# Optimization experiments

Measured on AMD Instinct MI355X. Metric: run time of the kernel, lower is better.

The kernel has to match this reference:

```python
import jax, jax.numpy as jnp
import numpy as np

B, S, E, H = 4, 2048, 1024, 16
DH = E // H  # head_dim = 64


def setup_inputs() -> dict:
    key = jax.random.key(0)
    k1, k2, k3 = jax.random.split(key, 3)
    x = jax.random.normal(k1, (B, S, E), dtype=jnp.float32)
    # xavier-uniform-like scale for dense kernels
    Wqkv = jax.random.normal(k2, (E, 3 * E), dtype=jnp.float32) * (1.0 / np.sqrt(E))
    Wout = jax.random.normal(k3, (E, E), dtype=jnp.float32) * (1.0 / np.sqrt(E))
    return {"x": x, "Wqkv": Wqkv, "Wout": Wout}


def reference(x, Wqkv, Wout):
    b, s, e = x.shape
    qkv = jnp.einsum("bse,ef->bsf", x, Wqkv)            # [B,S,3E]
    qkv = qkv.reshape(b, s, H, 3 * DH).transpose(0, 2, 1, 3)  # [B,H,S,3*DH]
    q, k, v = jnp.split(qkv, 3, axis=-1)                # each [B,H,S,DH]
    scale = 1.0 / jnp.sqrt(jnp.asarray(DH, dtype=x.dtype))
    scores = jnp.einsum("bhqd,bhkd->bhqk", q, k) * scale  # [B,H,S,S] materialized
    attn = jax.nn.softmax(scores, axis=-1)
    values = jnp.einsum("bhqk,bhkd->bhqd", attn, v)     # [B,H,S,DH]
    values = values.transpose(0, 2, 1, 3).reshape(b, s, e)
    out = jnp.einsum("bse,ef->bsf", values, Wout)       # [B,S,E]
    return out
```

## Files before the change

### kernel.cpp

```cpp
#include <hip/hip_runtime.h>

typedef __attribute__((ext_vector_type(8))) __bf16 bf16x8;
typedef __attribute__((ext_vector_type(4))) float f32x4;

#define LOG2E 1.4426950408889634f
#define QSCALE (0.125f * LOG2E)

static __device__ __forceinline__ void gl_lds16(const void* g, void* l) {
  __builtin_amdgcn_global_load_lds(
      (__attribute__((address_space(1))) void*)(g),
      (__attribute__((address_space(3))) void*)(l), 16, 0, 0);
}

__global__ __launch_bounds__(256) void convert_f32_bf16(const float* __restrict__ in,
                                                        __bf16* __restrict__ out,
                                                        int n8) {
  const int i = blockIdx.x * 256 + threadIdx.x;
  if (i >= n8) return;
  const f32x4 a = *(const f32x4*)(in + (size_t)i * 8);
  const f32x4 b = *(const f32x4*)(in + (size_t)i * 8 + 4);
  bf16x8 o;
#pragma unroll
  for (int j = 0; j < 4; ++j) o[j] = (__bf16)a[j];
#pragma unroll
  for (int j = 0; j < 4; ++j) o[4 + j] = (__bf16)b[j];
  *(bf16x8*)(out + (size_t)i * 8) = o;
}

__global__ __launch_bounds__(256) void transpose_f32_bf16(
    const float* __restrict__ in, __bf16* __restrict__ out, int R, int C) {
  __shared__ __bf16 tile[64][72];
  const int t = threadIdx.x;
  const int c0 = blockIdx.x * 64;
  const int r0 = blockIdx.y * 64;
  const int lr = t >> 2;
  const int lc = (t & 3) * 16;
  const float* src = in + (size_t)(r0 + lr) * C + c0 + lc;
  bf16x8 w0, w1;
#pragma unroll
  for (int j = 0; j < 2; ++j) {
    const f32x4 a = *(const f32x4*)(src + j * 8);
    const f32x4 b = *(const f32x4*)(src + j * 8 + 4);
    bf16x8 o;
#pragma unroll
    for (int k = 0; k < 4; ++k) o[k] = (__bf16)a[k];
#pragma unroll
    for (int k = 0; k < 4; ++k) o[4 + k] = (__bf16)b[k];
    *(bf16x8*)&tile[lr][lc + j * 8] = o;
  }
  __syncthreads();
#pragma unroll
  for (int j = 0; j < 8; ++j) {
    w0[j] = tile[lc + j][lr];
    w1[j] = tile[lc + 8 + j][lr];
  }
  __bf16* dst = out + (size_t)(c0 + lr) * R + r0 + lc;
  *(bf16x8*)dst = w0;
  *(bf16x8*)(dst + 8) = w1;
}


#define STAGE_A(TT, KH)                                                  \
  do {                                                                   \
    const int kg_ = (TT) * 64 + (KH) * 32;                               \
    char* d_ = lds + ((TT) & 1) * 32768 + (KH) * 16384 + t * 16;         \
    gl_lds16(Ab + g0 + kg_, d_);                                         \
    gl_lds16(Ab + g1 + kg_, d_ + 8192);                                  \
  } while (0)

#define STAGE_B(TT, KH)                                                  \
  do {                                                                   \
    const int kg_ = (TT) * 64 + (KH) * 32;                               \
    char* d_ = lds + 65536 + ((TT) & 1) * 16384 + (KH) * 8192 + t * 16;  \
    gl_lds16(Bb + g0 + kg_, d_);                                         \
  } while (0)

#define READ_AB(KK)                                                              \
  do {                                                                           \
    const char* pa_ = lds + buf * 32768 + (KK) * 16384 + wm * 8192 + lfo;        \
    a0 = *(const bf16x8*)pa_;                                                    \
    a1 = *(const bf16x8*)(pa_ + 1024);                                           \
    a2 = *(const bf16x8*)(pa_ + 2048);                                           \
    a3 = *(const bf16x8*)(pa_ + 3072);                                           \
    a4 = *(const bf16x8*)(pa_ + 4096);                                           \
    a5 = *(const bf16x8*)(pa_ + 5120);                                           \
    a6 = *(const bf16x8*)(pa_ + 6144);                                           \
    a7 = *(const bf16x8*)(pa_ + 7168);                                           \
    const char* pb_ = lds + 65536 + buf * 16384 + (KK) * 8192 + wn * 2048 + lfo; \
    b0 = *(const bf16x8*)pb_;                                                    \
    b1 = *(const bf16x8*)(pb_ + 1024);                                           \
  } while (0)

#define MROW(MI, AV)                                                             \
  acc[MI][0] = __builtin_amdgcn_mfma_f32_16x16x32_bf16(AV, b0, acc[MI][0], 0, 0, 0); \
  acc[MI][1] = __builtin_amdgcn_mfma_f32_16x16x32_bf16(AV, b1, acc[MI][1], 0, 0, 0);

#define MFMA16()                       \
  do {                                 \
    __builtin_amdgcn_s_setprio(1);     \
    MROW(0, a0)                        \
    MROW(1, a1)                        \
    MROW(2, a2)                        \
    MROW(3, a3)                        \
    MROW(4, a4)                        \
    MROW(5, a5)                        \
    MROW(6, a6)                        \
    MROW(7, a7)                        \
    __builtin_amdgcn_s_setprio(0);     \
  } while (0)

template <int EPI>
__global__ __launch_bounds__(512, 2) void gemm256(
    const __bf16* __restrict__ A, const __bf16* __restrict__ Bt,
    float* __restrict__ Cf, __bf16* __restrict__ q_ws, __bf16* __restrict__ k_ws,
    __bf16* __restrict__ vT_ws, int M, int N, int K) {
  (void)M;
  extern __shared__ char lds[];
  const int t = threadIdx.x;
  const int lane = t & 63;
  const int quad = lane >> 4, l15 = lane & 15;
  const int w = t >> 6;
  const int wm = w >> 2, wn = w & 3;

  const int olid = blockIdx.y * gridDim.x + blockIdx.x;
  const int xcd = olid & 7, loc = olid >> 3;
  const int m0 = (xcd * 4 + (loc & 3)) * 256;
  const int n0 = (loc >> 2) * 128;

  int rowS[2], kcS[2];
#pragma unroll
  for (int l = 0; l < 2; ++l) {
    const int LB = l * 8192 + t * 16;
    const int r_in = (LB >> 6) & 15;
    const int ch = ((LB >> 5) & 1) ^ ((r_in >> 3) & 1);
    rowS[l] = (LB >> 10) * 16 + r_in;
    kcS[l] = ch * 16 + ((LB >> 4) & 1) * 8;
  }
  const __bf16* Ab = A + (size_t)m0 * K;
  const __bf16* Bb = Bt + (size_t)n0 * K;
  const size_t g0 = (size_t)rowS[0] * K + kcS[0];
  const size_t g1 = (size_t)rowS[1] * K + kcS[1];

  const int lfo = l15 * 64 + ((((quad >> 1) ^ (l15 >> 3)) & 1) << 5) + ((quad & 1) << 4);

  const f32x4 fzero = {0.f, 0.f, 0.f, 0.f};
  f32x4 acc[8][2];
#pragma unroll
  for (int i = 0; i < 8; ++i) {
    acc[i][0] = fzero;
    acc[i][1] = fzero;
  }

  const int nt = K >> 6;
  bf16x8 a0, a1, a2, a3, a4, a5, a6, a7, b0, b1;

  STAGE_A(0, 0);
  STAGE_B(0, 0);
  STAGE_A(0, 1);
  STAGE_B(0, 1);
  if (nt > 1) {
    STAGE_A(1, 0);
    STAGE_B(1, 0);
    asm volatile("s_waitcnt vmcnt(3)");
  } else {
    asm volatile("s_waitcnt vmcnt(0)");
  }
  __builtin_amdgcn_s_barrier();

  for (int tt = 0; tt < nt; ++tt) {
    const int buf = tt & 1;
    READ_AB(0);
    if (tt + 1 < nt) {
      STAGE_A(tt + 1, 1);
      STAGE_B(tt + 1, 1);
    }
    __builtin_amdgcn_s_barrier();
    asm volatile("s_waitcnt lgkmcnt(0)");
    MFMA16();
    if (tt + 1 < nt)
      asm volatile("s_waitcnt vmcnt(6)");
    else
      asm volatile("s_waitcnt vmcnt(0)");
    __builtin_amdgcn_s_barrier();
    READ_AB(1);
    if (tt + 2 < nt) {
      STAGE_A(tt + 2, 0);
      STAGE_B(tt + 2, 0);
    }
    __builtin_amdgcn_s_barrier();
    asm volatile("s_waitcnt lgkmcnt(0)");
    MFMA16();
    if (tt + 2 < nt)
      asm volatile("s_waitcnt vmcnt(6)");
    else if (tt + 1 < nt)
      asm volatile("s_waitcnt vmcnt(3)");
    else
      asm volatile("s_waitcnt vmcnt(0)");
    __builtin_amdgcn_s_barrier();
  }

#pragma unroll
  for (int mi = 0; mi < 8; ++mi) {
#pragma unroll
    for (int r = 0; r < 4; ++r) {
      const int row = m0 + wm * 128 + mi * 16 + quad * 4 + r;
#pragma unroll
      for (int ni = 0; ni < 2; ++ni) {
        const int col = n0 + wn * 32 + ni * 16 + l15;
        const float v = acc[mi][ni][r];
        if (EPI == 0) {
          const int b = row >> 11, s = row & 2047;
          const int h = col / 192;
          const int rr = col - h * 192;
          const int ty = rr >> 6, d = rr & 63;
          const int bh = b * 16 + h;
          if (ty == 0)
            q_ws[((size_t)bh * 2048 + s) * 64 + d] = (__bf16)(v * QSCALE);
          else if (ty == 1)
            k_ws[((size_t)bh * 2048 + s) * 64 + d] = (__bf16)v;
          else
            vT_ws[((size_t)bh * 64 + d) * 2048 + s] = (__bf16)v;
        } else {
          Cf[(size_t)row * N + col] = v;
        }
      }
    }
  }
}

__global__ __launch_bounds__(256) void flash_attn(
    const __bf16* __restrict__ q_ws, const __bf16* __restrict__ k_ws,
    const __bf16* __restrict__ vT_ws, __bf16* __restrict__ values, int bh0) {
  __shared__ __bf16 sK[64][72];
  __shared__ __bf16 sVt[64][72];
  __shared__ __bf16 sP[4][32][72];
  const int t = threadIdx.x;
  const int lane = t & 63, w = t >> 6, quad = lane >> 4, l15 = lane & 15;
  const int qt = blockIdx.x;
  const int bh = blockIdx.y + bh0;
  const __bf16* Qb = q_ws + (size_t)bh * 2048 * 64;
  const __bf16* Kb = k_ws + (size_t)bh * 2048 * 64;
  const __bf16* Vtb = vT_ws + (size_t)bh * 64 * 2048;
  const int qrow0 = qt * 128 + w * 32;

  bf16x8 qf[2][2];
#pragma unroll
  for (int mi = 0; mi < 2; ++mi)
#pragma unroll
    for (int ks = 0; ks < 2; ++ks)
      qf[mi][ks] = *(const bf16x8*)(Qb + (size_t)(qrow0 + mi * 16 + l15) * 64 +
                                    ks * 32 + quad * 8);

  bf16x8 ones;
#pragma unroll
  for (int j = 0; j < 8; ++j) ones[j] = (__bf16)1.0f;

  const f32x4 fzero = {0.f, 0.f, 0.f, 0.f};
  f32x4 accO[2][4];
  f32x4 accL[2];
#pragma unroll
  for (int mi = 0; mi < 2; ++mi) {
    accL[mi] = fzero;
#pragma unroll
    for (int ni = 0; ni < 4; ++ni) accO[mi][ni] = fzero;
  }

  const int srow = t >> 2;
  const int scol = (t & 3) * 16;

  bf16x8 ka, kb2, va, vb;
  {
    const __bf16* ks0 = Kb + (size_t)srow * 64 + scol;
    ka = *(const bf16x8*)ks0;
    kb2 = *(const bf16x8*)(ks0 + 8);
    const __bf16* vs0 = Vtb + (size_t)srow * 2048 + scol;
    va = *(const bf16x8*)vs0;
    vb = *(const bf16x8*)(vs0 + 8);
  }

  for (int kt = 0; kt < 32; ++kt) {
    *(bf16x8*)&sK[srow][scol] = ka;
    *(bf16x8*)&sK[srow][scol + 8] = kb2;
    *(bf16x8*)&sVt[srow][scol] = va;
    *(bf16x8*)&sVt[srow][scol + 8] = vb;
    __syncthreads();

    if (kt < 31) {
      const __bf16* ksn = Kb + (size_t)((kt + 1) * 64 + srow) * 64 + scol;
      ka = *(const bf16x8*)ksn;
      kb2 = *(const bf16x8*)(ksn + 8);
      const __bf16* vsn = Vtb + (size_t)srow * 2048 + (kt + 1) * 64 + scol;
      va = *(const bf16x8*)vsn;
      vb = *(const bf16x8*)(vsn + 8);
    }

    f32x4 accS[2][4];
#pragma unroll
    for (int mi = 0; mi < 2; ++mi)
#pragma unroll
      for (int ni = 0; ni < 4; ++ni) accS[mi][ni] = fzero;
#pragma unroll
    for (int ks = 0; ks < 2; ++ks) {
      bf16x8 kf[4];
#pragma unroll
      for (int ni = 0; ni < 4; ++ni)
        kf[ni] = *(const bf16x8*)&sK[ni * 16 + l15][ks * 32 + quad * 8];
#pragma unroll
      for (int mi = 0; mi < 2; ++mi)
#pragma unroll
        for (int ni = 0; ni < 4; ++ni)
          accS[mi][ni] = __builtin_amdgcn_mfma_f32_16x16x32_bf16(
              qf[mi][ks], kf[ni], accS[mi][ni], 0, 0, 0);
    }

#pragma unroll
    for (int mi = 0; mi < 2; ++mi) {
#pragma unroll
      for (int r = 0; r < 4; ++r) {
        const int prow = mi * 16 + quad * 4 + r;
#pragma unroll
        for (int ni = 0; ni < 4; ++ni) {
          const float p = __builtin_amdgcn_exp2f(accS[mi][ni][r]);
          sP[w][prow][ni * 16 + l15] = (__bf16)p;
        }
      }
    }
    __threadfence_block();

#pragma unroll
    for (int ks = 0; ks < 2; ++ks) {
      bf16x8 vf[4], pf[2];
#pragma unroll
      for (int ni = 0; ni < 4; ++ni)
        vf[ni] = *(const bf16x8*)&sVt[ni * 16 + l15][ks * 32 + quad * 8];
#pragma unroll
      for (int mi = 0; mi < 2; ++mi)
        pf[mi] = *(const bf16x8*)&sP[w][mi * 16 + l15][ks * 32 + quad * 8];
#pragma unroll
      for (int mi = 0; mi < 2; ++mi) {
#pragma unroll
        for (int ni = 0; ni < 4; ++ni)
          accO[mi][ni] = __builtin_amdgcn_mfma_f32_16x16x32_bf16(
              pf[mi], vf[ni], accO[mi][ni], 0, 0, 0);
        accL[mi] = __builtin_amdgcn_mfma_f32_16x16x32_bf16(pf[mi], ones, accL[mi],
                                                           0, 0, 0);
      }
    }
    __syncthreads();
  }

  const int b = bh >> 4, h = bh & 15;
#pragma unroll
  for (int mi = 0; mi < 2; ++mi) {
#pragma unroll
    for (int r = 0; r < 4; ++r) {
      const float inv = 1.0f / accL[mi][r];
      const int s = qrow0 + mi * 16 + quad * 4 + r;
#pragma unroll
      for (int ni = 0; ni < 4; ++ni)
        values[((size_t)(b * 2048 + s)) * 1024 + h * 64 + ni * 16 + l15] =
            (__bf16)(accO[mi][ni][r] * inv);
    }
  }
}

extern "C" void kernel_launch(void* const* d_in, const int* in_sizes, int n_in,
                              void* d_out, int out_size, void* d_ws, size_t ws_size,
                              hipStream_t stream) {
  (void)out_size; (void)ws_size;
  float* out = (float*)d_out;
  char* wsb = (char*)d_ws;
  __bf16* xb = (__bf16*)(wsb + 256);
  __bf16* WqkvT = xb + 8388608;
  __bf16* WoutT = WqkvT + 3145728;
  __bf16* q_ws = WoutT + 1048576;
  __bf16* k_ws = q_ws + 8388608;
  __bf16* vT_ws = k_ws + 8388608;
  __bf16* values = xb;

  const float *px = (const float*)d_in[0], *pw = (const float*)d_in[1],
              *po = (const float*)d_in[2];
  for (int i = 0; i < n_in; ++i) {
    if (in_sizes[i] == 8388608) px = (const float*)d_in[i];
    else if (in_sizes[i] == 3145728) pw = (const float*)d_in[i];
    else if (in_sizes[i] == 1048576) po = (const float*)d_in[i];
  }

  hipFuncSetAttribute(reinterpret_cast<const void*>(&gemm256<0>),
                      hipFuncAttributeMaxDynamicSharedMemorySize, 98304);
  hipFuncSetAttribute(reinterpret_cast<const void*>(&gemm256<1>),
                      hipFuncAttributeMaxDynamicSharedMemorySize, 98304);

  convert_f32_bf16<<<4096, 256, 0, stream>>>(px, xb, 1048576);
  transpose_f32_bf16<<<dim3(48, 16), 256, 0, stream>>>(pw, WqkvT, 1024, 3072);
  transpose_f32_bf16<<<dim3(16, 16), 256, 0, stream>>>(po, WoutT, 1024, 1024);
  gemm256<0><<<dim3(32, 24), 512, 98304, stream>>>(xb, WqkvT, nullptr, q_ws, k_ws,
                                                   vT_ws, 8192, 3072, 1024);
  flash_attn<<<dim3(16, 64), 256, 0, stream>>>(q_ws, k_ws, vT_ws, values, 0);
  gemm256<1><<<dim3(32, 8), 512, 98304, stream>>>(values, WoutT, out, nullptr,
                                                  nullptr, nullptr, 8192, 1024, 1024);
}
```

Measured before the change: 310.0 us.

## Shrink GEMM tile to 128x128, split attention launch, change sP padding

The GEMM kernel's M tile drops from 256 to 128 rows. Each warp now holds four MFMA rows instead of eight, LDS use falls to 64KB, and the launch bounds ask for 4 blocks per CU, so twice as many blocks run with higher occupancy. The cost is less data reuse per block. Separately, the flash attention launch is split into two launches of 32 heads each. The sP row padding changes from 72 to 68, which alters the LDS bank mapping and could add conflicts or affect alignment.

```diff
diff --git a/kernel.cpp b/kernel.cpp
--- a/kernel.cpp
+++ b/kernel.cpp
@@ -62,31 +62,24 @@
 
 #define STAGE_A(TT, KH)                                                  \
   do {                                                                   \
-    const int kg_ = (TT) * 64 + (KH) * 32;                               \
-    char* d_ = lds + ((TT) & 1) * 32768 + (KH) * 16384 + t * 16;         \
-    gl_lds16(Ab + g0 + kg_, d_);                                         \
-    gl_lds16(Ab + g1 + kg_, d_ + 8192);                                  \
+    char* d_ = lds + ((TT) & 1) * 16384 + (KH) * 8192 + t * 16;          \
+    gl_lds16(Ab + gsrc + (TT) * 64 + (KH) * 32, d_);                     \
   } while (0)
 
 #define STAGE_B(TT, KH)                                                  \
   do {                                                                   \
-    const int kg_ = (TT) * 64 + (KH) * 32;                               \
-    char* d_ = lds + 65536 + ((TT) & 1) * 16384 + (KH) * 8192 + t * 16;  \
-    gl_lds16(Bb + g0 + kg_, d_);                                         \
+    char* d_ = lds + 32768 + ((TT) & 1) * 16384 + (KH) * 8192 + t * 16;  \
+    gl_lds16(Bb + gsrc + (TT) * 64 + (KH) * 32, d_);                     \
   } while (0)
 
 #define READ_AB(KK)                                                              \
   do {                                                                           \
-    const char* pa_ = lds + buf * 32768 + (KK) * 16384 + wm * 8192 + lfo;        \
+    const char* pa_ = lds + buf * 16384 + (KK) * 8192 + wm * 4096 + lfo;         \
     a0 = *(const bf16x8*)pa_;                                                    \
     a1 = *(const bf16x8*)(pa_ + 1024);                                           \
     a2 = *(const bf16x8*)(pa_ + 2048);                                           \
     a3 = *(const bf16x8*)(pa_ + 3072);                                           \
-    a4 = *(const bf16x8*)(pa_ + 4096);                                           \
-    a5 = *(const bf16x8*)(pa_ + 5120);                                           \
-    a6 = *(const bf16x8*)(pa_ + 6144);                                           \
-    a7 = *(const bf16x8*)(pa_ + 7168);                                           \
-    const char* pb_ = lds + 65536 + buf * 16384 + (KK) * 8192 + wn * 2048 + lfo; \
+    const char* pb_ = lds + 32768 + buf * 16384 + (KK) * 8192 + wn * 2048 + lfo; \
     b0 = *(const bf16x8*)pb_;                                                    \
     b1 = *(const bf16x8*)(pb_ + 1024);                                           \
   } while (0)
@@ -95,22 +88,18 @@
   acc[MI][0] = __builtin_amdgcn_mfma_f32_16x16x32_bf16(AV, b0, acc[MI][0], 0, 0, 0); \
   acc[MI][1] = __builtin_amdgcn_mfma_f32_16x16x32_bf16(AV, b1, acc[MI][1], 0, 0, 0);
 
-#define MFMA16()                       \
+#define MFMA8()                        \
   do {                                 \
     __builtin_amdgcn_s_setprio(1);     \
     MROW(0, a0)                        \
     MROW(1, a1)                        \
     MROW(2, a2)                        \
     MROW(3, a3)                        \
-    MROW(4, a4)                        \
-    MROW(5, a5)                        \
-    MROW(6, a6)                        \
-    MROW(7, a7)                        \
     __builtin_amdgcn_s_setprio(0);     \
   } while (0)
 
 template <int EPI>
-__global__ __launch_bounds__(512, 2) void gemm256(
+__global__ __launch_bounds__(512, 4) void gemm128(
     const __bf16* __restrict__ A, const __bf16* __restrict__ Bt,
     float* __restrict__ Cf, __bf16* __restrict__ q_ws, __bf16* __restrict__ k_ws,
     __bf16* __restrict__ vT_ws, int M, int N, int K) {
@@ -124,35 +113,30 @@
 
   const int olid = blockIdx.y * gridDim.x + blockIdx.x;
   const int xcd = olid & 7, loc = olid >> 3;
-  const int m0 = (xcd * 4 + (loc & 3)) * 256;
-  const int n0 = (loc >> 2) * 128;
-
-  int rowS[2], kcS[2];
-#pragma unroll
-  for (int l = 0; l < 2; ++l) {
-    const int LB = l * 8192 + t * 16;
-    const int r_in = (LB >> 6) & 15;
-    const int ch = ((LB >> 5) & 1) ^ ((r_in >> 3) & 1);
-    rowS[l] = (LB >> 10) * 16 + r_in;
-    kcS[l] = ch * 16 + ((LB >> 4) & 1) * 8;
-  }
+  const int m0 = (xcd * 8 + (loc & 7)) * 128;
+  const int n0 = (loc >> 3) * 128;
+
+  const int LB = t * 16;
+  const int r_in = (LB >> 6) & 15;
+  const int ch = ((LB >> 5) & 1) ^ ((r_in >> 3) & 1);
+  const int rowS = (LB >> 10) * 16 + r_in;
+  const int kcS = ch * 16 + ((LB >> 4) & 1) * 8;
   const __bf16* Ab = A + (size_t)m0 * K;
   const __bf16* Bb = Bt + (size_t)n0 * K;
-  const size_t g0 = (size_t)rowS[0] * K + kcS[0];
-  const size_t g1 = (size_t)rowS[1] * K + kcS[1];
+  const size_t gsrc = (size_t)rowS * K + kcS;
 
   const int lfo = l15 * 64 + ((((quad >> 1) ^ (l15 >> 3)) & 1) << 5) + ((quad & 1) << 4);
 
   const f32x4 fzero = {0.f, 0.f, 0.f, 0.f};
-  f32x4 acc[8][2];
-#pragma unroll
-  for (int i = 0; i < 8; ++i) {
+  f32x4 acc[4][2];
+#pragma unroll
+  for (int i = 0; i < 4; ++i) {
     acc[i][0] = fzero;
     acc[i][1] = fzero;
   }
 
   const int nt = K >> 6;
-  bf16x8 a0, a1, a2, a3, a4, a5, a6, a7, b0, b1;
+  bf16x8 a0, a1, a2, a3, b0, b1;
 
   STAGE_A(0, 0);
   STAGE_B(0, 0);
@@ -161,7 +145,7 @@
   if (nt > 1) {
     STAGE_A(1, 0);
     STAGE_B(1, 0);
-    asm volatile("s_waitcnt vmcnt(3)");
+    asm volatile("s_waitcnt vmcnt(4)");
   } else {
     asm volatile("s_waitcnt vmcnt(0)");
   }
@@ -176,9 +160,9 @@
     }
     __builtin_amdgcn_s_barrier();
     asm volatile("s_waitcnt lgkmcnt(0)");
-    MFMA16();
+    MFMA8();
     if (tt + 1 < nt)
-      asm volatile("s_waitcnt vmcnt(6)");
+      asm volatile("s_waitcnt vmcnt(4)");
     else
       asm volatile("s_waitcnt vmcnt(0)");
     __builtin_amdgcn_s_barrier();
@@ -189,21 +173,21 @@
     }
     __builtin_amdgcn_s_barrier();
     asm volatile("s_waitcnt lgkmcnt(0)");
-    MFMA16();
+    MFMA8();
     if (tt + 2 < nt)
-      asm volatile("s_waitcnt vmcnt(6)");
+      asm volatile("s_waitcnt vmcnt(4)");
     else if (tt + 1 < nt)
-      asm volatile("s_waitcnt vmcnt(3)");
+      asm volatile("s_waitcnt vmcnt(2)");
     else
       asm volatile("s_waitcnt vmcnt(0)");
     __builtin_amdgcn_s_barrier();
   }
 
 #pragma unroll
-  for (int mi = 0; mi < 8; ++mi) {
+  for (int mi = 0; mi < 4; ++mi) {
 #pragma unroll
     for (int r = 0; r < 4; ++r) {
-      const int row = m0 + wm * 128 + mi * 16 + quad * 4 + r;
+      const int row = m0 + wm * 64 + mi * 16 + quad * 4 + r;
 #pragma unroll
       for (int ni = 0; ni < 2; ++ni) {
         const int col = n0 + wn * 32 + ni * 16 + l15;
@@ -233,7 +217,7 @@
     const __bf16* __restrict__ vT_ws, __bf16* __restrict__ values, int bh0) {
   __shared__ __bf16 sK[64][72];
   __shared__ __bf16 sVt[64][72];
-  __shared__ __bf16 sP[4][32][72];
+  __shared__ __bf16 sP[4][32][68];
   const int t = threadIdx.x;
   const int lane = t & 63, w = t >> 6, quad = lane >> 4, l15 = lane & 15;
   const int qt = blockIdx.x;
@@ -386,17 +370,18 @@
     else if (in_sizes[i] == 1048576) po = (const float*)d_in[i];
   }
 
-  hipFuncSetAttribute(reinterpret_cast<const void*>(&gemm256<0>),
-                      hipFuncAttributeMaxDynamicSharedMemorySize, 98304);
-  hipFuncSetAttribute(reinterpret_cast<const void*>(&gemm256<1>),
-                      hipFuncAttributeMaxDynamicSharedMemorySize, 98304);
+  hipFuncSetAttribute(reinterpret_cast<const void*>(&gemm128<0>),
+                      hipFuncAttributeMaxDynamicSharedMemorySize, 65536);
+  hipFuncSetAttribute(reinterpret_cast<const void*>(&gemm128<1>),
+                      hipFuncAttributeMaxDynamicSharedMemorySize, 65536);
 
   convert_f32_bf16<<<4096, 256, 0, stream>>>(px, xb, 1048576);
   transpose_f32_bf16<<<dim3(48, 16), 256, 0, stream>>>(pw, WqkvT, 1024, 3072);
   transpose_f32_bf16<<<dim3(16, 16), 256, 0, stream>>>(po, WoutT, 1024, 1024);
-  gemm256<0><<<dim3(32, 24), 512, 98304, stream>>>(xb, WqkvT, nullptr, q_ws, k_ws,
+  gemm128<0><<<dim3(64, 24), 512, 65536, stream>>>(xb, WqkvT, nullptr, q_ws, k_ws,
                                                    vT_ws, 8192, 3072, 1024);
-  flash_attn<<<dim3(16, 64), 256, 0, stream>>>(q_ws, k_ws, vT_ws, values, 0);
-  gemm256<1><<<dim3(32, 8), 512, 98304, stream>>>(values, WoutT, out, nullptr,
+  flash_attn<<<dim3(16, 32), 256, 0, stream>>>(q_ws, k_ws, vT_ws, values, 0);
+  flash_attn<<<dim3(16, 32), 256, 0, stream>>>(q_ws, k_ws, vT_ws, values, 32);
+  gemm128<1><<<dim3(64, 8), 512, 65536, stream>>>(values, WoutT, out, nullptr,
                                                   nullptr, nullptr, 8192, 1024, 1024);
 }
```

Result: no change. 308.3 us (-0.5%).
